# Optimization experiments

Measured on AMD Instinct MI355X. Metric: run time of the kernel, lower is better.

Reference implementation:

```python
import jax, jax.numpy as jnp
import numpy as np

HIDDEN = 512
HEADS = 8
HEAD_DIM = HIDDEN // HEADS
MAX_DIST = 10
B, N = 16, 512
EPS = 1e-5


def _layer_norm(x, g, b):
    mu = jnp.mean(x, axis=-1, keepdims=True)
    var = jnp.mean(jnp.square(x - mu), axis=-1, keepdims=True)
    return (x - mu) * jax.lax.rsqrt(var + EPS) * g + b


def setup_inputs() -> dict:
    key = jax.random.key(0)
    ks = jax.random.split(key, 16)
    s = 0.02
    inp = {
        "x": jax.random.normal(ks[0], (B, N, HIDDEN), jnp.float32),
        "distances": jax.random.randint(ks[1], (B, N, N), 0, MAX_DIST, jnp.int32),
        "edge_features": jax.random.normal(ks[2], (B, N, N), jnp.float32),
        "attn_mask": jax.random.randint(ks[3], (B, N), 0, 2).astype(bool),
        "Wq": jax.random.normal(ks[4], (HIDDEN, HIDDEN), jnp.float32) * s,
        "bq": jnp.zeros((HIDDEN,), jnp.float32),
        "Wk": jax.random.normal(ks[5], (HIDDEN, HIDDEN), jnp.float32) * s,
        "bk": jnp.zeros((HIDDEN,), jnp.float32),
        "Wv": jax.random.normal(ks[6], (HIDDEN, HIDDEN), jnp.float32) * s,
        "bv": jnp.zeros((HIDDEN,), jnp.float32),
        "Wo": jax.random.normal(ks[7], (HIDDEN, HIDDEN), jnp.float32) * s,
        "bo": jnp.zeros((HIDDEN,), jnp.float32),
        "spatial_emb": jax.random.normal(ks[8], (MAX_DIST, HEADS), jnp.float32) * s,
        "edge_w": jax.random.normal(ks[9], (HEADS,), jnp.float32) * s,
        "edge_b": jnp.zeros((HEADS,), jnp.float32),
        "ln1_g": jnp.ones((HIDDEN,), jnp.float32),
        "ln1_b": jnp.zeros((HIDDEN,), jnp.float32),
        "ln2_g": jnp.ones((HIDDEN,), jnp.float32),
        "ln2_b": jnp.zeros((HIDDEN,), jnp.float32),
        "W1": jax.random.normal(ks[10], (HIDDEN, 4 * HIDDEN), jnp.float32) * s,
        "b1": jnp.zeros((4 * HIDDEN,), jnp.float32),
        "W2": jax.random.normal(ks[11], (4 * HIDDEN, HIDDEN), jnp.float32) * s,
        "b2": jnp.zeros((HIDDEN,), jnp.float32),
    }
    return inp


def reference(x, distances, edge_features, attn_mask, Wq, bq, Wk, bk, Wv, bv,
              Wo, bo, spatial_emb, edge_w, edge_b, ln1_g, ln1_b, ln2_g, ln2_b,
              W1, b1, W2, b2):
    b, n, _ = x.shape
    q = (x @ Wq + bq).reshape(b, n, HEADS, HEAD_DIM)
    k = (x @ Wk + bk).reshape(b, n, HEADS, HEAD_DIM)
    v = (x @ Wv + bv).reshape(b, n, HEADS, HEAD_DIM)
    # [b, h, i, j] attention scores
    scores = jnp.einsum('bihd,bjhd->bhij', q, k) / np.sqrt(HEAD_DIM).astype(np.float32)
    spatial_bias = spatial_emb[distances]                       # [b, i, j, h]
    edge_bias = edge_features[..., None] * edge_w + edge_b      # [b, i, j, h]
    scores = scores + jnp.transpose(spatial_bias + edge_bias, (0, 3, 1, 2))
    scores = jnp.where(attn_mask[:, None, None, :], -jnp.inf, scores)
    attn = jax.nn.softmax(scores, axis=-1)
    out = jnp.einsum('bhij,bjhd->bihd', attn, v).reshape(b, n, HIDDEN)
    out = out @ Wo + bo
    h = _layer_norm(x + out, ln1_g, ln1_b)
    ffn = jax.nn.relu(h @ W1 + b1) @ W2 + b2
    return _layer_norm(h + ffn, ln2_g, ln2_b)
```

## Files before the change

### kernel.cpp

```cpp
#include <hip/hip_runtime.h>
#include <stdint.h>
#include <stddef.h>

#define SEQ   512
#define HID   512
#define NHEAD 8
#define HD    64
#define NBATCH 16
#define NTOK  8192
#define MAXD  10
#define LOG2E 1.4426950408889634f

typedef __attribute__((ext_vector_type(8))) short short8;
typedef __attribute__((ext_vector_type(4))) float f32x4;

typedef __attribute__((address_space(3))) void        as3_void;
typedef const __attribute__((address_space(1))) void  as1_cvoid;

#define MFMA16(a,b,c) __builtin_amdgcn_mfma_f32_16x16x32_bf16((a),(b),(c),0,0,0)

__device__ __forceinline__ float bf2f(uint16_t u){ return __uint_as_float(((uint32_t)u)<<16); }
__device__ __forceinline__ uint16_t f2bf(float f){
  uint32_t i = __float_as_uint(f);
  return (uint16_t)((i + 0x7fffu + ((i>>16)&1u)) >> 16);
}
__device__ __forceinline__ uint16_t f2bf_rtz(float f){
  return (uint16_t)(__float_as_uint(f) >> 16);
}

enum { EPI_BF16=0, EPI_F32=3, EPI_RELU=4 };

__global__ __launch_bounds__(256) void prep_kernel(
    const float* __restrict__ x, uint16_t* __restrict__ xb,
    const float* __restrict__ Wq, const float* __restrict__ Wk,
    const float* __restrict__ Wv, const float* __restrict__ Wo,
    const float* __restrict__ W1, const float* __restrict__ W2,
    uint16_t* __restrict__ tq, uint16_t* __restrict__ tk,
    uint16_t* __restrict__ tv, uint16_t* __restrict__ to_,
    uint16_t* __restrict__ t1, uint16_t* __restrict__ t2)
{
  int id = blockIdx.x;
  if (id >= 3072){
    int i = (id-3072)*256 + threadIdx.x;
    if (i < NTOK*HID/4){
      float4 v = *(const float4*)(x + (size_t)i*4);
      *(ushort4*)(xb + (size_t)i*4) =
          make_ushort4(f2bf(v.x), f2bf(v.y), f2bf(v.z), f2bf(v.w));
    }
    return;
  }
  __shared__ uint16_t tile[32][33];
  const float* in; uint16_t* out; int R, C, tx, ty;
  if (id < 1024) {
    int m = id >> 8, loc = id & 255;
    in  = (m==0)?Wq:(m==1)?Wk:(m==2)?Wv:Wo;
    out = (m==0)?tq:(m==1)?tk:(m==2)?tv:to_;
    R = 512; C = 512; ty = loc>>4; tx = loc&15;
  } else if (id < 2048) {
    int loc = id-1024; in=W1; out=t1; R=512; C=2048; ty=loc>>6; tx=loc&63;
  } else {
    int loc = id-2048; in=W2; out=t2; R=2048; C=512; ty=loc>>4; tx=loc&15;
  }
  int bx = tx*32, by = ty*32;
  int lx = threadIdx.x & 31, ly = threadIdx.x >> 5;
  #pragma unroll
  for (int i=ly; i<32; i+=8) tile[i][lx] = f2bf(in[(size_t)(by+i)*C + bx+lx]);
  __syncthreads();
  #pragma unroll
  for (int i=ly; i<32; i+=8) out[(size_t)(bx+i)*R + by+lx] = tile[lx][i];
}

template<int BM, int BN>
__device__ __forceinline__ void gemm_tile_mainloop(
    const uint16_t* __restrict__ A, const uint16_t* __restrict__ Bt,
    int K, int m0, int n0, uint16_t* lA, uint16_t* lB,
    f32x4 acc[4][(BM==128)?4:((BN==128)?2:1)])
{
  constexpr int NJ  = (BM==128)?4:((BN==128)?2:1);
  constexpr int ARD = BM/32;
  constexpr int BRD = BN/32;
  const int t = threadIdx.x;
  const int w = t>>6, l = t&63;
  const int lg = l>>4, lc = l&15;
  const int wr = (BM==128)?(w>>1):0;
  const int wc = (BM==128)?(w&1):w;
  const int swz = lc & 7;
  const int kSteps = K>>6;

  auto stage = [&](int kt, int buf){
    const int k0 = kt<<6;
    #pragma unroll
    for (int rd=0; rd<ARD; ++rd){
      const int e   = rd*2048 + t*8;
      const int row = e>>6;
      const int col = (((e>>3)&7) ^ (row&7))*8;
      const uint16_t* ga = A + (size_t)(m0+row)*K + (k0+col);
      char* la = (char*)(lA + buf*(BM*64)) + rd*4096 + w*1024;
      __builtin_amdgcn_global_load_lds((as1_cvoid*)ga, (as3_void*)la, 16, 0, 0);
    }
    #pragma unroll
    for (int rd=0; rd<BRD; ++rd){
      const int e   = rd*2048 + t*8;
      const int row = e>>6;
      const int col = (((e>>3)&7) ^ (row&7))*8;
      const uint16_t* gb = Bt + (size_t)(n0+row)*K + (k0+col);
      char* lb = (char*)(lB + buf*(BN*64)) + rd*4096 + w*1024;
      __builtin_amdgcn_global_load_lds((as1_cvoid*)gb, (as3_void*)lb, 16, 0, 0);
    }
  };

  auto compute = [&](const uint16_t* rA, const uint16_t* rB){
    #pragma unroll
    for (int kk=0; kk<2; ++kk){
      const int cc = (kk*4 + lg) ^ swz;
      short8 af[4], bfr[NJ];
      #pragma unroll
      for (int i=0;i<4;i++)
        af[i]  = *(const short8*)&rA[(wr*64 + i*16 + lc)*64 + cc*8];
      #pragma unroll
      for (int j=0;j<NJ;j++)
        bfr[j] = *(const short8*)&rB[(wc*16*NJ + j*16 + lc)*64 + cc*8];
      #pragma unroll
      for (int i=0;i<4;i++)
        #pragma unroll
        for (int j=0;j<NJ;j++)
          acc[i][j] = MFMA16(af[i], bfr[j], acc[i][j]);
    }
  };

  stage(0, 0);
  __syncthreads();
  int cur = 0;
  for (int kt=0; kt<kSteps; ++kt){
    if (kt+1 < kSteps) stage(kt+1, cur^1);
    compute(lA + cur*(BM*64), lB + cur*(BN*64));
    __syncthreads();
    cur ^= 1;
  }
}

template<int EPI, int BM, int BN>
__global__ __launch_bounds__(256,2) void gemm_bt(
    const uint16_t* __restrict__ A, const uint16_t* __restrict__ Bt,
    const float* __restrict__ bias, void* __restrict__ outp,
    int M, int N, int K)
{
  constexpr int NJ = (BM==128)?4:((BN==128)?2:1);
  __shared__ uint16_t lA[2*BM*64];
  __shared__ uint16_t lB[2*BN*64];
  f32x4 acc[4][NJ];
  #pragma unroll
  for (int i=0;i<4;i++)
    #pragma unroll
    for (int j=0;j<NJ;j++){ f32x4 z = {0.f,0.f,0.f,0.f}; acc[i][j]=z; }
  const int m0 = blockIdx.x*BM, n0 = blockIdx.y*BN;
  gemm_tile_mainloop<BM,BN>(A, Bt, K, m0, n0, lA, lB, acc);

  const int t=threadIdx.x, w=t>>6, l=t&63, lg=l>>4, lc=l&15;
  const int wr=(BM==128)?(w>>1):0, wc=(BM==128)?(w&1):w;
  #pragma unroll
  for (int j=0;j<NJ;j++){
    const int col = n0 + wc*16*NJ + j*16 + lc;
    const float bs = bias[col];
    #pragma unroll
    for (int i=0;i<4;i++){
      const int rowb = m0 + wr*64 + i*16 + lg*4;
      #pragma unroll
      for (int r=0;r<4;r++){
        float v = acc[i][j][r] + bs;
        if constexpr (EPI==EPI_RELU)   v = fmaxf(v, 0.f);
        if constexpr (EPI==EPI_F32)
          ((float*)outp)[(size_t)(rowb+r)*N + col] = v;
        else
          ((uint16_t*)outp)[(size_t)(rowb+r)*N + col] = f2bf(v);
      }
    }
  }
}

__global__ __launch_bounds__(256,2) void qkv_pack(
    const uint16_t* __restrict__ x,
    const uint16_t* __restrict__ wtq, const uint16_t* __restrict__ wtk,
    const uint16_t* __restrict__ wtv,
    const float* __restrict__ bq, const float* __restrict__ bk,
    const float* __restrict__ bv,
    uint16_t* __restrict__ qo, uint16_t* __restrict__ kp,
    uint16_t* __restrict__ vp,
    const int*   __restrict__ dist,
    const float* __restrict__ edge,
    const int*   __restrict__ mask,
    uint32_t*    __restrict__ biasp)
{
  __shared__ char smem[2*2*128*64*2];
  const int t = threadIdx.x;
  const int flat = blockIdx.x + 64*(blockIdx.y + 4*blockIdx.z);

  if ((flat & 3) == 3){
    int*   dl = (int*)smem;
    float* el = (float*)(smem + 16*260*4);
    int*   ml = (int*)(smem + 2*16*260*4);
    #define DL(r,c) dl[(r)*260+(c)]
    #define EL(r,c) el[(r)*260+(c)]
    #pragma unroll
    for (int u0=0; u0<2; ++u0){
      const int u  = (flat>>2)*2 + u0;
      const int b  = u>>5, it = u&31;
      __syncthreads();
      ml[t]     = mask[b*SEQ + t];
      ml[t+256] = mask[b*SEQ + t + 256];
      #pragma unroll
      for (int jh=0; jh<2; ++jh){
        if (jh) __syncthreads();
        {
          const int r  = t >> 4;
          const int c0 = (t & 15) * 16;
          const size_t g = ((size_t)b*SEQ + it*16 + r)*SEQ + jh*256 + c0;
          *(int4*)&DL(r,c0)      = *(const int4*)&dist[g];
          *(int4*)&DL(r,c0+4)    = *(const int4*)&dist[g+4];
          *(int4*)&DL(r,c0+8)    = *(const int4*)&dist[g+8];
          *(int4*)&DL(r,c0+12)   = *(const int4*)&dist[g+12];
          *(float4*)&EL(r,c0)    = *(const float4*)&edge[g];
          *(float4*)&EL(r,c0+4)  = *(const float4*)&edge[g+4];
          *(float4*)&EL(r,c0+8)  = *(const float4*)&edge[g+8];
          *(float4*)&EL(r,c0+12) = *(const float4*)&edge[g+12];
        }
        __syncthreads();
        {
          const int i   = t & 15;
          const int j0p = (t >> 4) * 16;
          const int jn  = (j0p >> 4) & 3;
          const int jt  = jh*4 + (j0p >> 6);
          uint32_t wv[16];
          #pragma unroll
          for (int e=0; e<16; ++e){
            const int jl = j0p + e;
            const int jg = jh*256 + jl;
            const uint32_t d  = (uint32_t)DL(i,jl) & 0xFFu;
            const uint32_t mk = (ml[jg] ? 1u : 0u) << 8;
            wv[e] = ((uint32_t)f2bf(EL(i,jl)) << 16) | mk | d;
          }
          uint32_t* ob = biasp + ((((size_t)b*32 + it)*8 + jt)*64)*16;
          #pragma unroll
          for (int lgq=0; lgq<4; ++lgq)
            *(uint4*)&ob[(lgq*16 + i)*16 + jn*4] =
                make_uint4(wv[lgq*4], wv[lgq*4+1], wv[lgq*4+2], wv[lgq*4+3]);
        }
      }
    }
    #undef DL
    #undef EL
    return;
  }

  const int g  = (flat>>2)*3 + (flat&3);
  const int m0 = (g & 63) * 128;
  const int n0 = ((g >> 6) & 3) * 128;
  const int z  = g >> 8;
  uint16_t* lA = (uint16_t*)smem;
  uint16_t* lB = lA + 2*128*64;
  const uint16_t* Bt = (z==0)?wtq:(z==1)?wtk:wtv;
  const float*  bias = (z==0)?bq :(z==1)?bk :bv;
  f32x4 acc[4][4];
  #pragma unroll
  for (int i=0;i<4;i++)
    #pragma unroll
    for (int j=0;j<4;j++){ f32x4 zz = {0.f,0.f,0.f,0.f}; acc[i][j]=zz; }
  gemm_tile_mainloop<128,128>(x, Bt, HID, m0, n0, lA, lB, acc);

  const int w=t>>6, l=t&63, lg=l>>4, lc=l&15, wr=w>>1, wc=w&1;
  if (z==0){
    const float scale = 0.125f * LOG2E;
    #pragma unroll
    for (int j=0;j<4;j++){
      const int col = n0 + wc*64 + j*16 + lc;
      const float bs = bias[col];
      #pragma unroll
      for (int i=0;i<4;i++){
        const int rowb = m0 + wr*64 + i*16 + lg*4;
        #pragma unroll
        for (int r=0;r<4;r++)
          qo[(size_t)(rowb+r)*HID + col] = f2bf((acc[i][j][r] + bs)*scale);
      }
    }
  } else if (z==1){
    #pragma unroll
    for (int j=0;j<4;j++){
      const int col = n0 + wc*64 + j*16 + lc;
      const float bs = bias[col];
      const int h_ = col>>6, cm = col&63, kk = cm>>5, lgk = (cm>>3)&3, e = col&7;
      #pragma unroll
      for (int i=0;i<4;i++){
        const int rowb = m0 + wr*64 + i*16 + lg*4;
        #pragma unroll
        for (int r=0;r<4;r++){
          const int tok = rowb + r;
          const int b_ = tok>>9, tl = tok&511;
          const int jt = tl>>6, jn = (tl>>4)&3, lck = tl&15;
          kp[((((size_t)(b_*8+h_)*8 + jt)*4 + jn)*2 + kk)*512
             + (lgk*16 + lck)*8 + e] = f2bf(acc[i][j][r] + bs);
        }
      }
    }
  } else {
    #pragma unroll
    for (int j=0;j<4;j++){
      const int col = n0 + wc*64 + j*16 + lc;
      const float bs = bias[col];
      const int h_ = col>>6, dn = (col>>4)&3, lcv = col&15;
      #pragma unroll
      for (int i=0;i<4;i++){
        const int rowb = m0 + wr*64 + i*16 + lg*4;
        const int b_ = rowb>>9, tl = rowb&511;
        const int jt = tl>>6, kk = (tl>>5)&1, lgv = (tl>>3)&3, e0 = tl&7;
        *(ushort4*)&vp[((((size_t)(b_*8+h_)*8 + jt)*2 + kk)*4 + dn)*512
                       + (lgv*16 + lcv)*8 + e0] =
            make_ushort4(f2bf(acc[i][j][0]+bs), f2bf(acc[i][j][1]+bs),
                         f2bf(acc[i][j][2]+bs), f2bf(acc[i][j][3]+bs));
      }
    }
  }
}

__global__ __launch_bounds__(512,4) void attn_kernel(
    const uint16_t* __restrict__ q,
    const uint16_t* __restrict__ kp,
    const uint16_t* __restrict__ vp,
    const uint32_t* __restrict__ biasp,
    const float*    __restrict__ semb,
    const float*    __restrict__ ew,
    const float*    __restrict__ eb,
    uint16_t* __restrict__ out)
{
  __shared__ float sp_rep[NHEAD][64][11];
  __shared__ uint16_t plds[NHEAD][2][16*64];
  const int b  = blockIdx.y;
  const int it = blockIdx.x;
  const int i0 = it*16;
  const int t  = threadIdx.x;
  const int h  = t>>6, l = t&63, lg = l>>4, lc = l&15;
  for (int i = t; i < NHEAD*64*MAXD; i += 512){
    const int hh = i / (64*MAXD), rem = i % (64*MAXD);
    const int a = rem / MAXD, d = rem % MAXD;
    sp_rep[hh][a][d] = (semb[d*NHEAD + hh] + eb[hh]) * LOG2E;
  }
  __syncthreads();
  const float ewf = ew[h] * LOG2E;
  const float* spl = &sp_rep[h][l][0];
  char* pbase = (char*)&plds[h][0][0];
  const int swz = (lc&7)<<4;

  short8 qf[2];
  #pragma unroll
  for (int kk=0;kk<2;kk++)
    qf[kk] = *(const short8*)&q[(size_t)(b*SEQ + i0 + lc)*HID + h*HD + kk*32 + lg*8];

  const uint4* bp = (const uint4*)(biasp + (((size_t)b*32 + it)*8)*64*16);
  const uint16_t* kpb = kp + (size_t)(b*8+h)*8*4*2*512 + l*8;
  const uint16_t* vpb = vp + (size_t)(b*8+h)*8*2*4*512 + l*8;

  float mrun[2] = {-1e30f, -1e30f};
  float lrun[2] = {0.f, 0.f};
  f32x4 oacc[2][4];
  #pragma unroll
  for (int s=0;s<2;s++)
    #pragma unroll
    for (int dn=0;dn<4;dn++){ f32x4 z={0.f,0.f,0.f,0.f}; oacc[s][dn]=z; }

  #pragma unroll
  for (int p=0; p<4; ++p){
    #pragma unroll
    for (int s=0; s<2; ++s){
      const int jt = s*4 + p;
      uint32_t uw[16];
      {
        const uint4* bq_ = bp + (jt*64 + l)*4;
        *(uint4*)&uw[0]  = bq_[0];
        *(uint4*)&uw[4]  = bq_[1];
        *(uint4*)&uw[8]  = bq_[2];
        *(uint4*)&uw[12] = bq_[3];
      }
      f32x4 st[4];
      #pragma unroll
      for (int jn=0;jn<4;jn++){ f32x4 z={0.f,0.f,0.f,0.f}; st[jn]=z; }
      __builtin_amdgcn_s_setprio(1);
      #pragma unroll
      for (int jn=0;jn<4;jn++){
        #pragma unroll
        for (int kk=0;kk<2;kk++){
          short8 kf = *(const short8*)&kpb[(size_t)((jt*4 + jn)*2 + kk)*512];
          st[jn] = MFMA16(kf, qf[kk], st[jn]);
        }
      }
      __builtin_amdgcn_s_setprio(0);
      float tmax = -1e30f;
      #pragma unroll
      for (int jn=0;jn<4;jn++){
        #pragma unroll
        for (int r=0;r<4;r++){
          const uint32_t u = uw[jn*4+r];
          float sv = st[jn][r] + spl[u & 0xFFu]
                   + bf2f((uint16_t)(u >> 16))*ewf;
          if (u & 0x100u) sv = -1e30f;
          st[jn][r] = sv;
          tmax = fmaxf(tmax, sv);
        }
      }
      {
        float tm = fmaxf(tmax, __shfl_xor(tmax, 16, 64));
        tm = fmaxf(tm, __shfl_xor(tm, 32, 64));
        float mnew = fmaxf(mrun[s], tm);
        mnew = fmaxf(mnew, -1e20f);
        const float c = __builtin_amdgcn_exp2f(mrun[s] - mnew);
        mrun[s] = mnew;
        float lsum = 0.f;
        char* pb = pbase + s*(16*64*2) + lc*128;
        #pragma unroll
        for (int jn=0;jn<4;jn++){
          float p0 = __builtin_amdgcn_exp2f(st[jn][0]-mnew);
          float p1 = __builtin_amdgcn_exp2f(st[jn][1]-mnew);
          float p2 = __builtin_amdgcn_exp2f(st[jn][2]-mnew);
          float p3 = __builtin_amdgcn_exp2f(st[jn][3]-mnew);
          lsum += (p0+p1)+(p2+p3);
          *(ushort4*)(pb + (((jn*16 + lg*4)*2) ^ swz)) =
              make_ushort4(f2bf_rtz(p0), f2bf_rtz(p1),
                           f2bf_rtz(p2), f2bf_rtz(p3));
        }
        lrun[s] = lrun[s]*c + lsum;
        #pragma unroll
        for (int r=0;r<4;r++){
          const float cr = __shfl(c, lg*4+r, 64);
          #pragma unroll
          for (int dn=0;dn<4;dn++) oacc[s][dn][r] *= cr;
        }
      }
    }
    #pragma unroll
    for (int s=0; s<2; ++s){
      const int jt = s*4 + p;
      char* pb = pbase + s*(16*64*2) + lc*128;
      __builtin_amdgcn_s_setprio(1);
      #pragma unroll
      for (int kk=0;kk<2;kk++){
        short8 pa = *(const short8*)(pb + (((kk*32 + lg*8)*2) ^ swz));
        #pragma unroll
        for (int dn=0;dn<4;dn++){
          short8 vb = *(const short8*)&vpb[(size_t)((jt*2 + kk)*4 + dn)*512];
          oacc[s][dn] = MFMA16(pa, vb, oacc[s][dn]);
        }
      }
      __builtin_amdgcn_s_setprio(0);
    }
  }
  {
    const float mm = fmaxf(mrun[0], mrun[1]);
    const float c0 = __builtin_amdgcn_exp2f(mrun[0]-mm);
    const float c1 = __builtin_amdgcn_exp2f(mrun[1]-mm);
    float ls = lrun[0]*c0 + lrun[1]*c1;
    ls += __shfl_xor(ls, 16, 64);
    ls += __shfl_xor(ls, 32, 64);
    const float inv = 1.f/ls;
    #pragma unroll
    for (int r=0;r<4;r++){
      const float cr0 = __shfl(c0, lg*4+r, 64);
      const float cr1 = __shfl(c1, lg*4+r, 64);
      const float ir  = __shfl(inv, lg*4+r, 64);
      const size_t orow = ((size_t)b*SEQ + i0 + lg*4 + r)*HID;
      #pragma unroll
      for (int dn=0;dn<4;dn++)
        out[orow + h*HD + dn*16 + lc] =
            f2bf((oacc[0][dn][r]*cr0 + oacc[1][dn][r]*cr1)*ir);
    }
  }
}

__global__ __launch_bounds__(256) void ln_kernel(
    const uint16_t* __restrict__ a, const uint16_t* __restrict__ bsrc,
    const float* __restrict__ g, const float* __restrict__ bb,
    float* __restrict__ of, uint16_t* __restrict__ ob)
{
  const int row = blockIdx.x*4 + (threadIdx.x>>6);
  const int l = threadIdx.x & 63;
  const int c0 = l*8;
  const uint16_t* ar = a    + (size_t)row*HID + c0;
  const uint16_t* br = bsrc + (size_t)row*HID + c0;
  short8 av = *(const short8*)ar;
  short8 bv = *(const short8*)br;
  float u[8];
  #pragma unroll
  for (int e=0;e<8;e++)
    u[e] = bf2f((uint16_t)av[e]) + bf2f((uint16_t)bv[e]);
  float s=0.f, ss=0.f;
  #pragma unroll
  for (int e=0;e<8;e++){ s += u[e]; ss += u[e]*u[e]; }
  #pragma unroll
  for (int off=32; off>=1; off>>=1){
    s  += __shfl_xor(s,  off, 64);
    ss += __shfl_xor(ss, off, 64);
  }
  const float mu  = s*(1.f/512.f);
  const float inv = rsqrtf(ss*(1.f/512.f) - mu*mu + 1e-5f);
  float4 g0 = *(const float4*)(g + c0),  g1 = *(const float4*)(g + c0 + 4);
  float4 q0 = *(const float4*)(bb + c0), q1 = *(const float4*)(bb + c0 + 4);
  float y[8];
  y[0]=(u[0]-mu)*inv*g0.x+q0.x; y[1]=(u[1]-mu)*inv*g0.y+q0.y;
  y[2]=(u[2]-mu)*inv*g0.z+q0.z; y[3]=(u[3]-mu)*inv*g0.w+q0.w;
  y[4]=(u[4]-mu)*inv*g1.x+q1.x; y[5]=(u[5]-mu)*inv*g1.y+q1.y;
  y[6]=(u[6]-mu)*inv*g1.z+q1.z; y[7]=(u[7]-mu)*inv*g1.w+q1.w;
  if (of){
    float* orow = of + (size_t)row*HID + c0;
    *(float4*)orow     = make_float4(y[0],y[1],y[2],y[3]);
    *(float4*)(orow+4) = make_float4(y[4],y[5],y[6],y[7]);
  }
  if (ob){
    uint16_t* brow = ob + (size_t)row*HID + c0;
    *(ushort4*)brow     = make_ushort4(f2bf(y[0]),f2bf(y[1]),f2bf(y[2]),f2bf(y[3]));
    *(ushort4*)(brow+4) = make_ushort4(f2bf(y[4]),f2bf(y[5]),f2bf(y[6]),f2bf(y[7]));
  }
}

extern "C" void kernel_launch(void* const* d_in, const int* in_sizes, int n_in,
                              void* d_out, int out_size, void* d_ws, size_t ws_size,
                              hipStream_t stream)
{
  (void)in_sizes; (void)n_in; (void)out_size; (void)ws_size;
  const float* x    = (const float*)d_in[0];
  const int*   dist = (const int*)  d_in[1];
  const float* edge = (const float*)d_in[2];
  const int*   mask = (const int*)  d_in[3];
  const float* Wq = (const float*)d_in[4];
  const float* bq = (const float*)d_in[5];
  const float* Wk = (const float*)d_in[6];
  const float* bk = (const float*)d_in[7];
  const float* Wv = (const float*)d_in[8];
  const float* bv = (const float*)d_in[9];
  const float* Wo = (const float*)d_in[10];
  const float* bo = (const float*)d_in[11];
  const float* semb = (const float*)d_in[12];
  const float* ew   = (const float*)d_in[13];
  const float* eb   = (const float*)d_in[14];
  const float* ln1g = (const float*)d_in[15];
  const float* ln1b = (const float*)d_in[16];
  const float* ln2g = (const float*)d_in[17];
  const float* ln2b = (const float*)d_in[18];
  const float* W1 = (const float*)d_in[19];
  const float* b1 = (const float*)d_in[20];
  const float* W2 = (const float*)d_in[21];
  const float* b2 = (const float*)d_in[22];

  char* ws = (char*)d_ws;
  uint16_t* xb16  = (uint16_t*)ws;
  uint16_t* qbuf  = xb16  + (size_t)NTOK*HID;
  uint16_t* kpbuf = qbuf  + (size_t)NTOK*HID;
  uint16_t* vpbuf = kpbuf + (size_t)NTOK*HID;
  uint16_t* aobuf = vpbuf + (size_t)NTOK*HID;
  uint16_t* f1buf = qbuf;
  uint32_t* biasp = (uint32_t*)(ws + (size_t)5*NTOK*HID*2);
  uint16_t* tb16  = (uint16_t*)biasp;
  uint16_t* t2b16 = tb16;
  uint16_t* hb16  = (uint16_t*)((char*)biasp + (size_t)NTOK*HID*4);
  uint16_t* wt    = hb16 + (size_t)NTOK*HID;
  uint16_t* wtq = wt;
  uint16_t* wtk = wtq + 512*512;
  uint16_t* wtv = wtk + 512*512;
  uint16_t* wto = wtv + 512*512;
  uint16_t* wt1 = wto + 512*512;
  uint16_t* wt2 = wt1 + 512*2048;

  prep_kernel<<<7168, 256, 0, stream>>>(x, xb16, Wq,Wk,Wv,Wo,W1,W2,
                                        wtq,wtk,wtv,wto,wt1,wt2);

  qkv_pack<<<dim3(64,4,4), 256, 0, stream>>>(xb16, wtq,wtk,wtv, bq,bk,bv,
                                             qbuf, kpbuf, vpbuf,
                                             dist, edge, mask, biasp);

  attn_kernel<<<dim3(32,16), 512, 0, stream>>>(qbuf, kpbuf, vpbuf, biasp,
                                               semb, ew, eb, aobuf);

  gemm_bt<EPI_BF16,64,128><<<dim3(128,4), 256, 0, stream>>>(aobuf, wto, bo, tb16, NTOK, HID, HID);

  ln_kernel<<<2048, 256, 0, stream>>>(tb16, xb16, ln1g, ln1b, nullptr, hb16);

  gemm_bt<EPI_RELU,128,128><<<dim3(64,16), 256, 0, stream>>>(hb16, wt1, b1, f1buf, NTOK, 2048, HID);

  gemm_bt<EPI_BF16,64,128><<<dim3(128,4), 256, 0, stream>>>(f1buf, wt2, b2, t2b16, NTOK, HID, 2048);

  ln_kernel<<<2048, 256, 0, stream>>>(t2b16, hb16, ln2g, ln2b, (float*)d_out, nullptr);
}
```

Before: 153.1 us.

## Process attention keys in 128-wide chunks with single online-softmax stream

Replaces the two interleaved 64-key online-softmax streams (with their own running max, sum and output accumulators, merged at the end) with a single stream that handles 128 keys per step. Each step computes eight score tiles, does one max/rescale pass, writes a 128-wide P tile into shared memory, and runs the PV MFMAs over four k-slices. This halves the number of rescale and shuffle passes and drops the final merge of the two streams. In exchange it loses the overlap between the two independent streams and raises register pressure from eight live score tiles.

Measured after the change: 154.6 us. About the same (+1.0%).

```diff
diff --git a/kernel.cpp b/kernel.cpp
--- a/kernel.cpp
+++ b/kernel.cpp
@@ -332,7 +332,7 @@
     uint16_t* __restrict__ out)
 {
   __shared__ float sp_rep[NHEAD][64][11];
-  __shared__ uint16_t plds[NHEAD][2][16*64];
+  __shared__ uint16_t plds[NHEAD][16*128];
   const int b  = blockIdx.y;
   const int it = blockIdx.x;
   const int i0 = it*16;
@@ -346,7 +346,7 @@
   __syncthreads();
   const float ewf = ew[h] * LOG2E;
   const float* spl = &sp_rep[h][l][0];
-  char* pbase = (char*)&plds[h][0][0];
+  char* pb = (char*)&plds[h][0] + lc*256;
   const int swz = (lc&7)<<4;
 
   short8 qf[2];
@@ -358,117 +358,103 @@
   const uint16_t* kpb = kp + (size_t)(b*8+h)*8*4*2*512 + l*8;
   const uint16_t* vpb = vp + (size_t)(b*8+h)*8*2*4*512 + l*8;
 
-  float mrun[2] = {-1e30f, -1e30f};
-  float lrun[2] = {0.f, 0.f};
-  f32x4 oacc[2][4];
-  #pragma unroll
-  for (int s=0;s<2;s++)
-    #pragma unroll
-    for (int dn=0;dn<4;dn++){ f32x4 z={0.f,0.f,0.f,0.f}; oacc[s][dn]=z; }
-
-  #pragma unroll
-  for (int p=0; p<4; ++p){
-    #pragma unroll
-    for (int s=0; s<2; ++s){
-      const int jt = s*4 + p;
+  float mrun = -1e30f;
+  float lrun = 0.f;
+  f32x4 oacc[4];
+  #pragma unroll
+  for (int dn=0;dn<4;dn++){ f32x4 z={0.f,0.f,0.f,0.f}; oacc[dn]=z; }
+
+  #pragma unroll
+  for (int jt128=0; jt128<4; ++jt128){
+    f32x4 st[8];
+    #pragma unroll
+    for (int jnn=0;jnn<8;jnn++){ f32x4 z={0.f,0.f,0.f,0.f}; st[jnn]=z; }
+    __builtin_amdgcn_s_setprio(1);
+    #pragma unroll
+    for (int jnn=0;jnn<8;jnn++){
+      #pragma unroll
+      for (int kk=0;kk<2;kk++){
+        short8 kf = *(const short8*)&kpb[(size_t)((jt128*8 + jnn)*2 + kk)*512];
+        st[jnn] = MFMA16(kf, qf[kk], st[jnn]);
+      }
+    }
+    __builtin_amdgcn_s_setprio(0);
+    float tmax = -1e30f;
+    #pragma unroll
+    for (int half=0; half<2; ++half){
       uint32_t uw[16];
       {
-        const uint4* bq_ = bp + (jt*64 + l)*4;
+        const uint4* bq_ = bp + ((jt128*2 + half)*64 + l)*4;
         *(uint4*)&uw[0]  = bq_[0];
         *(uint4*)&uw[4]  = bq_[1];
         *(uint4*)&uw[8]  = bq_[2];
         *(uint4*)&uw[12] = bq_[3];
       }
-      f32x4 st[4];
-      #pragma unroll
-      for (int jn=0;jn<4;jn++){ f32x4 z={0.f,0.f,0.f,0.f}; st[jn]=z; }
-      __builtin_amdgcn_s_setprio(1);
       #pragma unroll
       for (int jn=0;jn<4;jn++){
-        #pragma unroll
-        for (int kk=0;kk<2;kk++){
-          short8 kf = *(const short8*)&kpb[(size_t)((jt*4 + jn)*2 + kk)*512];
-          st[jn] = MFMA16(kf, qf[kk], st[jn]);
-        }
-      }
-      __builtin_amdgcn_s_setprio(0);
-      float tmax = -1e30f;
-      #pragma unroll
-      for (int jn=0;jn<4;jn++){
+        const int jnn = half*4 + jn;
         #pragma unroll
         for (int r=0;r<4;r++){
           const uint32_t u = uw[jn*4+r];
-          float sv = st[jn][r] + spl[u & 0xFFu]
+          float sv = st[jnn][r] + spl[u & 0xFFu]
                    + bf2f((uint16_t)(u >> 16))*ewf;
           if (u & 0x100u) sv = -1e30f;
-          st[jn][r] = sv;
+          st[jnn][r] = sv;
           tmax = fmaxf(tmax, sv);
         }
       }
-      {
-        float tm = fmaxf(tmax, __shfl_xor(tmax, 16, 64));
-        tm = fmaxf(tm, __shfl_xor(tm, 32, 64));
-        float mnew = fmaxf(mrun[s], tm);
-        mnew = fmaxf(mnew, -1e20f);
-        const float c = __builtin_amdgcn_exp2f(mrun[s] - mnew);
-        mrun[s] = mnew;
-        float lsum = 0.f;
-        char* pb = pbase + s*(16*64*2) + lc*128;
+    }
+    {
+      float tm = fmaxf(tmax, __shfl_xor(tmax, 16, 64));
+      tm = fmaxf(tm, __shfl_xor(tm, 32, 64));
+      float mnew = fmaxf(mrun, tm);
+      mnew = fmaxf(mnew, -1e20f);
+      const float c = __builtin_amdgcn_exp2f(mrun - mnew);
+      mrun = mnew;
+      float lsum = 0.f;
+      #pragma unroll
+      for (int jnn=0;jnn<8;jnn++){
+        float p0 = __builtin_amdgcn_exp2f(st[jnn][0]-mnew);
+        float p1 = __builtin_amdgcn_exp2f(st[jnn][1]-mnew);
+        float p2 = __builtin_amdgcn_exp2f(st[jnn][2]-mnew);
+        float p3 = __builtin_amdgcn_exp2f(st[jnn][3]-mnew);
+        lsum += (p0+p1)+(p2+p3);
+        *(ushort4*)(pb + ((jnn*32 + lg*8) ^ swz)) =
+            make_ushort4(f2bf_rtz(p0), f2bf_rtz(p1),
+                         f2bf_rtz(p2), f2bf_rtz(p3));
+      }
+      lrun = lrun*c + lsum;
+      #pragma unroll
+      for (int r=0;r<4;r++){
+        const float cr = __shfl(c, lg*4+r, 64);
         #pragma unroll
-        for (int jn=0;jn<4;jn++){
-          float p0 = __builtin_amdgcn_exp2f(st[jn][0]-mnew);
-          float p1 = __builtin_amdgcn_exp2f(st[jn][1]-mnew);
-          float p2 = __builtin_amdgcn_exp2f(st[jn][2]-mnew);
-          float p3 = __builtin_amdgcn_exp2f(st[jn][3]-mnew);
-          lsum += (p0+p1)+(p2+p3);
-          *(ushort4*)(pb + (((jn*16 + lg*4)*2) ^ swz)) =
-              make_ushort4(f2bf_rtz(p0), f2bf_rtz(p1),
-                           f2bf_rtz(p2), f2bf_rtz(p3));
-        }
-        lrun[s] = lrun[s]*c + lsum;
-        #pragma unroll
-        for (int r=0;r<4;r++){
-          const float cr = __shfl(c, lg*4+r, 64);
-          #pragma unroll
-          for (int dn=0;dn<4;dn++) oacc[s][dn][r] *= cr;
-        }
-      }
-    }
-    #pragma unroll
-    for (int s=0; s<2; ++s){
-      const int jt = s*4 + p;
-      char* pb = pbase + s*(16*64*2) + lc*128;
-      __builtin_amdgcn_s_setprio(1);
-      #pragma unroll
-      for (int kk=0;kk<2;kk++){
-        short8 pa = *(const short8*)(pb + (((kk*32 + lg*8)*2) ^ swz));
-        #pragma unroll
-        for (int dn=0;dn<4;dn++){
-          short8 vb = *(const short8*)&vpb[(size_t)((jt*2 + kk)*4 + dn)*512];
-          oacc[s][dn] = MFMA16(pa, vb, oacc[s][dn]);
-        }
-      }
-      __builtin_amdgcn_s_setprio(0);
-    }
+        for (int dn=0;dn<4;dn++) oacc[dn][r] *= cr;
+      }
+    }
+    __builtin_amdgcn_s_setprio(1);
+    #pragma unroll
+    for (int ks=0;ks<4;ks++){
+      short8 pa = *(const short8*)(pb + ((ks*64 + lg*16) ^ swz));
+      #pragma unroll
+      for (int dn=0;dn<4;dn++){
+        short8 vb = *(const short8*)&vpb[(size_t)((jt128*4 + ks)*4 + dn)*512];
+        oacc[dn] = MFMA16(pa, vb, oacc[dn]);
+      }
+    }
+    __builtin_amdgcn_s_setprio(0);
   }
   {
-    const float mm = fmaxf(mrun[0], mrun[1]);
-    const float c0 = __builtin_amdgcn_exp2f(mrun[0]-mm);
-    const float c1 = __builtin_amdgcn_exp2f(mrun[1]-mm);
-    float ls = lrun[0]*c0 + lrun[1]*c1;
+    float ls = lrun;
     ls += __shfl_xor(ls, 16, 64);
     ls += __shfl_xor(ls, 32, 64);
     const float inv = 1.f/ls;
     #pragma unroll
     for (int r=0;r<4;r++){
-      const float cr0 = __shfl(c0, lg*4+r, 64);
-      const float cr1 = __shfl(c1, lg*4+r, 64);
-      const float ir  = __shfl(inv, lg*4+r, 64);
+      const float ir = __shfl(inv, lg*4+r, 64);
       const size_t orow = ((size_t)b*SEQ + i0 + lg*4 + r)*HID;
       #pragma unroll
       for (int dn=0;dn<4;dn++)
-        out[orow + h*HD + dn*16 + lc] =
-            f2bf((oacc[0][dn][r]*cr0 + oacc[1][dn][r]*cr1)*ir);
+        out[orow + h*HD + dn*16 + lc] = f2bf(oacc[dn][r]*ir);
     }
   }
 }
```
